# Kernel optimization log

Hardware: AMD Instinct MI355X
Metric: run time of the kernel (lower is better)

Reference implementation:

```python
import jax, jax.numpy as jnp
import numpy as np

VOCAB = 50257
EMBED = 1024

def setup_inputs() -> dict:
    key = jax.random.key(0)
    k1, k2 = jax.random.split(key)
    hidden_states = jax.random.normal(k1, (2, 2048, EMBED), dtype=jnp.float32)
    # nn.Linear weight: [vocab_size, embed_dim], no bias
    W = jax.random.normal(k2, (VOCAB, EMBED), dtype=jnp.float32) * (1.0 / np.sqrt(EMBED))
    return {"hidden_states": hidden_states, "W": W}

def reference(hidden_states, W):
    # logits: [B, S, V] = hidden @ W^T
    logits = jnp.einsum("bsd,vd->bsv", hidden_states, W)
    return jax.nn.log_softmax(logits, axis=-1)
```

## Files before the change

kernel.cpp:

```cpp
#include <hip/hip_runtime.h>
#include <hip/hip_bf16.h>
#include <math.h>

#define VOCAB 50257
#define VPAD  50432
#define EMB   1024
#define NROWS 4096

#define BM 256
#define BN 256
#define BK 64
#define NKT (EMB / BK)
#define NMT (NROWS / BM)
#define NT  (VPAD / BN)
#define NWG (NMT * NT)

typedef __attribute__((ext_vector_type(4))) float  f32x4;
typedef __attribute__((ext_vector_type(16))) float f32x16;
typedef __attribute__((ext_vector_type(4), aligned(4))) float f32x4u;
typedef __attribute__((ext_vector_type(8))) __bf16 bf16x8;

#define FENCE asm volatile("" ::: "memory")
#define BARRIER do { FENCE; __builtin_amdgcn_s_barrier(); FENCE; } while (0)

__global__ __launch_bounds__(256)
void cvt_frag(const float* __restrict__ src, __bf16* __restrict__ dst,
              int valid_rows) {
    const long o8 = (long)blockIdx.x * 256 + threadIdx.x;
    const int l    = (int)(o8 & 63);
    const int u    = (int)((o8 >> 6) & 31);
    const int kt   = (int)((o8 >> 11) & 15);
    const int pn   = (int)(o8 >> 15);
    const int ks   = u >> 3, rblk = u & 7;
    const int grow = pn * 256 + rblk * 32 + (l & 31);
    const int gk   = kt * 64 + ks * 16 + (l >> 5) * 8;
    bf16x8 v;
    if (grow < valid_rows) {
        const float* p = src + (size_t)grow * EMB + gk;
        f32x4 a = *(const f32x4*)p;
        f32x4 b = *(const f32x4*)(p + 4);
        #pragma unroll
        for (int e = 0; e < 4; ++e) {
            v[e]     = (__bf16)a[e];
            v[4 + e] = (__bf16)b[e];
        }
    } else {
        #pragma unroll
        for (int e = 0; e < 8; ++e) v[e] = (__bf16)0.0f;
    }
    *(bf16x8*)(dst + o8 * 8) = v;
}

template <bool LB_OUT>
__global__ __launch_bounds__(512, 2)
void gemm_fused(const __bf16* __restrict__ A, const __bf16* __restrict__ B,
                float* __restrict__ C, __bf16* __restrict__ Lb,
                float* __restrict__ pbuf) {
    __shared__ alignas(16) __bf16 S[65536];

    const int tid  = threadIdx.x;
    const int lane = tid & 63;
    const int wave = tid >> 6;
    const int wm   = (wave >> 2) * 128;
    const int wn   = (wave & 3) * 64;
    const int l31  = lane & 31;
    const int h    = lane >> 5;

    const int b  = blockIdx.x;
    const int lg = (b & 7) * (NWG / 8) + (b >> 3);
    const int q  = lg >> 4, w = lg & 15;
    int mt, nt;
    if (q == 196) { mt = w; nt = 196; }
    else { mt = (q & 1) * 8 + (w & 7); nt = (q >> 1) * 2 + (w >> 3); }
    const int mtB = mt * BM, ntB = nt * BN;

    const __bf16* gAf = A + (size_t)mt * (16 * 16384) + lane * 8;
    const __bf16* gBf = B + (size_t)nt * (16 * 16384) + lane * 8;

    f32x16 acc[4][2];
    #pragma unroll
    for (int mb = 0; mb < 4; ++mb)
        #pragma unroll
        for (int nb = 0; nb < 2; ++nb)
            #pragma unroll
            for (int e = 0; e < 16; ++e) acc[mb][nb][e] = 0.0f;

#define GLOAD(gp, dp)                                                         \
    __builtin_amdgcn_global_load_lds(                                         \
        (const __attribute__((address_space(1))) void*)(gp),                 \
        (__attribute__((address_space(3))) void*)(dp), 16, 0, 0)

#define STAGE_A(bc, kt, u)                                                    \
    GLOAD(gAf + ((size_t)(kt) * 32 + (u) * 8 + wave) * 512,                   \
          &S[(bc) * 32768 + ((u) * 8 + wave) * 512])

#define STAGE_B(bc, kt, u)                                                    \
    GLOAD(gBf + ((size_t)(kt) * 32 + (u) * 8 + wave) * 512,                   \
          &S[(bc) * 32768 + 16384 + ((u) * 8 + wave) * 512])

#define LDA32(dst, c, ks) { _Pragma("unroll")                                 \
    for (int mb_ = 0; mb_ < 4; ++mb_)                                         \
        dst[mb_] = *(const bf16x8*)&S[(c) * 32768                            \
            + (((ks) * 8) + ((wm >> 5) + mb_)) * 512 + lane * 8]; }

#define LDB32(dst, c, ks) { _Pragma("unroll")                                 \
    for (int nb_ = 0; nb_ < 2; ++nb_)                                         \
        dst[nb_] = *(const bf16x8*)&S[(c) * 32768 + 16384                    \
            + (((ks) * 8) + ((wn >> 5) + nb_)) * 512 + lane * 8]; }

#define MFMA8(AF, BF)                                                         \
    __builtin_amdgcn_s_setprio(1);                                            \
    _Pragma("unroll") for (int mb_ = 0; mb_ < 4; ++mb_)                       \
        _Pragma("unroll") for (int nb_ = 0; nb_ < 2; ++nb_)                   \
            acc[mb_][nb_] = __builtin_amdgcn_mfma_f32_32x32x16_bf16(          \
                AF[mb_], BF[nb_], acc[mb_][nb_], 0, 0, 0);                    \
    __builtin_amdgcn_s_setprio(0);

    bf16x8 afA[4], afB[4], bfrA[2], bfrB[2];

    #pragma unroll
    for (int u = 0; u < 4; ++u) { STAGE_A(0, 0, u); STAGE_B(0, 0, u); }

    #pragma unroll 2
    for (int t = 0; t < NKT; ++t) {
        const int c = t & 1;
        const bool pf = (t + 1 < NKT);
        if (pf) {
            STAGE_A(c ^ 1, t + 1, 0); STAGE_B(c ^ 1, t + 1, 0);
            STAGE_A(c ^ 1, t + 1, 1); STAGE_B(c ^ 1, t + 1, 1);
            asm volatile("s_waitcnt vmcnt(4)" ::: "memory");
        } else {
            asm volatile("s_waitcnt vmcnt(0)" ::: "memory");
        }
        BARRIER;
        LDB32(bfrA, c, 0); LDA32(afA, c, 0);
        LDB32(bfrB, c, 1); LDA32(afB, c, 1);
        MFMA8(afA, bfrA);
        if (pf) { STAGE_A(c ^ 1, t + 1, 2); STAGE_B(c ^ 1, t + 1, 2); }
        LDB32(bfrA, c, 2); LDA32(afA, c, 2);
        MFMA8(afB, bfrB);
        if (pf) { STAGE_A(c ^ 1, t + 1, 3); STAGE_B(c ^ 1, t + 1, 3); }
        LDB32(bfrB, c, 3); LDA32(afB, c, 3);
        MFMA8(afA, bfrA);
        MFMA8(afB, bfrB);
        BARRIER;
    }
#undef STAGE_A
#undef STAGE_B
#undef GLOAD

    __syncthreads();
    const bool edge = (ntB + BN > VOCAB);

    if (LB_OUT) {
        #pragma unroll
        for (int mb = 0; mb < 4; ++mb) {
            #pragma unroll
            for (int r = 0; r < 16; ++r) {
                const int grow = mtB + wm + mb * 32 + (r & 3) + 8 * (r >> 2) + 4 * h;
                const size_t rb = (size_t)grow * VPAD + ntB + wn + l31;
                Lb[rb]      = (__bf16)acc[mb][0][r];
                Lb[rb + 32] = (__bf16)acc[mb][1][r];
            }
        }
    } else {
        #pragma unroll
        for (int mb = 0; mb < 4; ++mb) {
            #pragma unroll
            for (int r = 0; r < 16; ++r) {
                const int grow = mtB + wm + mb * 32 + (r & 3) + 8 * (r >> 2) + 4 * h;
                const size_t rb = (size_t)grow * VOCAB;
                const int col0 = ntB + wn + l31;
                if (!edge || col0 < VOCAB)      C[rb + col0]      = acc[mb][0][r];
                if (!edge || col0 + 32 < VOCAB) C[rb + col0 + 32] = acc[mb][1][r];
            }
        }
    }

    float* ldsP = (float*)&S[0];
    const int col0 = ntB + wn + l31;
    #pragma unroll
    for (int mb = 0; mb < 4; ++mb) {
        #pragma unroll
        for (int r = 0; r < 16; ++r) {
            float s = 0.0f;
            if (!edge || col0 < VOCAB)      s += __expf(acc[mb][0][r]);
            if (!edge || col0 + 32 < VOCAB) s += __expf(acc[mb][1][r]);
            s += __shfl_xor(s, 16);
            if (l31 < 16) {
                const int lrow = wm + mb * 32 + (r & 3) + 8 * (r >> 2) + 4 * h;
                ldsP[lrow * 68 + (wave & 3) * 16 + (lane & 15)] = s;
            }
        }
    }
    __syncthreads();

    {
        const int rl = tid >> 1, hf = tid & 1;
        const float* q2 = ldsP + rl * 68 + hf * 32;
        float s = 0.0f;
        #pragma unroll
        for (int k = 0; k < 8; ++k) {
            f32x4 v = *(const f32x4*)(q2 + k * 4);
            s += v[0] + v[1] + v[2] + v[3];
        }
        s += __shfl_xor(s, 1);
        if (hf == 0) pbuf[(size_t)nt * NROWS + mtB + rl] = s;
    }
}

__global__ __launch_bounds__(256)
void lse_reduce(const float* __restrict__ pbuf, float* __restrict__ lse) {
    __shared__ float sl[4][64];
    const int r0 = blockIdx.x * 64;
    const int l  = threadIdx.x & 63;
    const int w  = threadIdx.x >> 6;
    float s = 0.0f;
    for (int t = w; t < NT; t += 4)
        s += pbuf[(size_t)t * NROWS + r0 + l];
    sl[w][l] = s;
    __syncthreads();
    if (threadIdx.x < 64)
        lse[r0 + l] = __logf(sl[0][l] + sl[1][l] + sl[2][l] + sl[3][l]);
}

__global__ __launch_bounds__(256)
void expand_sub(const __bf16* __restrict__ Lb, const float* __restrict__ lse,
                float* __restrict__ C) {
    const int row = blockIdx.x >> 2;
    const int q   = blockIdx.x & 3;
    const float s = lse[row];
    const __bf16* src = Lb + (size_t)row * VPAD;
    float* dst = C + (size_t)row * VOCAB;
    const int i0 = q * 1571;
    const int i1 = (q == 3) ? 6282 : i0 + 1571;
    for (int i = i0 + threadIdx.x; i < i1; i += 256) {
        bf16x8 v = __builtin_nontemporal_load((const bf16x8*)(src + i * 8));
        f32x4u a, b2;
        a[0] = (float)v[0] - s; a[1] = (float)v[1] - s;
        a[2] = (float)v[2] - s; a[3] = (float)v[3] - s;
        b2[0] = (float)v[4] - s; b2[1] = (float)v[5] - s;
        b2[2] = (float)v[6] - s; b2[3] = (float)v[7] - s;
        __builtin_nontemporal_store(a,  (f32x4u*)(dst + i * 8));
        __builtin_nontemporal_store(b2, (f32x4u*)(dst + i * 8 + 4));
    }
    if (q == 3 && threadIdx.x == 0)
        dst[50256] = (float)src[50256] - s;
}

#define FBM 128
#define FBK 32
typedef __attribute__((ext_vector_type(4))) __bf16 bf16x4;
__device__ __forceinline__ int swz_idx(int row, int col) {
    int slot = (col >> 3) ^ ((row >> 1) & 3);
    return row * FBK + slot * 8 + (col & 7);
}

__global__ __launch_bounds__(256, 2)
void gemm_logits(const float* __restrict__ H, const float* __restrict__ W,
                 float* __restrict__ C) {
    __shared__ __bf16 ldsA[FBM * FBK];
    __shared__ __bf16 ldsB[FBM * FBK];

    const int tid  = threadIdx.x;
    const int lane = tid & 63;
    const int wave = tid >> 6;
    const int wm = (wave >> 1) * 64;
    const int wn = (wave & 1) * 64;
    const int mt = blockIdx.x;
    const int nt = blockIdx.y;
    const int srow = tid >> 1;
    const int scol = (tid & 1) * 16;
    const int brow_g = nt * FBM + srow;
    const bool bvalid = brow_g < VOCAB;
    const float* aptr = H + (size_t)(mt * FBM + srow) * EMB + scol;
    const float* bptr = W + (size_t)(bvalid ? brow_g : 0) * EMB + scol;

    f32x4 areg[4], breg[4];
    #pragma unroll
    for (int q = 0; q < 4; ++q) {
        areg[q] = *(const f32x4*)(aptr + q * 4);
        breg[q] = *(const f32x4*)(bptr + q * 4);
    }
    f32x4 acc[4][4];
    const f32x4 vzero = {0.f, 0.f, 0.f, 0.f};
    #pragma unroll
    for (int i = 0; i < 4; ++i)
        #pragma unroll
        for (int j = 0; j < 4; ++j) acc[i][j] = vzero;

    const int frow = lane & 15;
    const int kcol = (lane >> 4) * 8;

    for (int kt = 0; kt < EMB / FBK; ++kt) {
        __syncthreads();
        #pragma unroll
        for (int q = 0; q < 4; ++q) {
            const int col = scol + q * 4;
            bf16x4 av, bv;
            #pragma unroll
            for (int e = 0; e < 4; ++e) {
                av[e] = (__bf16)areg[q][e];
                bv[e] = bvalid ? (__bf16)breg[q][e] : (__bf16)0.0f;
            }
            *(bf16x4*)(&ldsA[swz_idx(srow, col)]) = av;
            *(bf16x4*)(&ldsB[swz_idx(srow, col)]) = bv;
        }
        __syncthreads();
        if (kt + 1 < EMB / FBK) {
            const int ko = (kt + 1) * FBK;
            #pragma unroll
            for (int q = 0; q < 4; ++q) {
                areg[q] = *(const f32x4*)(aptr + ko + q * 4);
                breg[q] = *(const f32x4*)(bptr + ko + q * 4);
            }
        }
        bf16x8 af[4], bfr[4];
        #pragma unroll
        for (int i = 0; i < 4; ++i) {
            af[i]  = *(const bf16x8*)(&ldsA[swz_idx(wm + i * 16 + frow, kcol)]);
            bfr[i] = *(const bf16x8*)(&ldsB[swz_idx(wn + i * 16 + frow, kcol)]);
        }
        #pragma unroll
        for (int i = 0; i < 4; ++i)
            #pragma unroll
            for (int j = 0; j < 4; ++j)
                acc[i][j] = __builtin_amdgcn_mfma_f32_16x16x32_bf16(
                    af[i], bfr[j], acc[i][j], 0, 0, 0);
    }

    const int crow = mt * FBM + wm + (lane >> 4) * 4;
    const int ccol = nt * FBM + wn + (lane & 15);
    #pragma unroll
    for (int i = 0; i < 4; ++i) {
        #pragma unroll
        for (int j = 0; j < 4; ++j) {
            const int col = ccol + j * 16;
            if (col < VOCAB) {
                #pragma unroll
                for (int r = 0; r < 4; ++r)
                    C[(size_t)(crow + i * 16 + r) * VOCAB + col] = acc[i][j][r];
            }
        }
    }
}

__global__ __launch_bounds__(256)
void row_lse(const float* __restrict__ C, float* __restrict__ lse) {
    const int row = blockIdx.x;
    const float* p = C + (size_t)row * VOCAB;

    float m = -INFINITY, l = 0.0f;
    for (int i = threadIdx.x; i < 12564; i += 256) {
        f32x4u v = *(const f32x4u*)(p + 4 * i);
        #pragma unroll
        for (int e = 0; e < 4; ++e) {
            const float x  = v[e];
            const float mn = fmaxf(m, x);
            l = l * __expf(m - mn) + __expf(x - mn);
            m = mn;
        }
    }
    if (threadIdx.x == 0) {
        const float x  = p[50256];
        const float mn = fmaxf(m, x);
        l = l * __expf(m - mn) + __expf(x - mn);
        m = mn;
    }
    #pragma unroll
    for (int off = 1; off < 64; off <<= 1) {
        const float mo = __shfl_xor(m, off);
        const float lo = __shfl_xor(l, off);
        const float mn = fmaxf(m, mo);
        l = l * __expf(m - mn) + lo * __expf(mo - mn);
        m = mn;
    }
    __shared__ float sm[4], sl[4];
    if ((threadIdx.x & 63) == 0) { sm[threadIdx.x >> 6] = m; sl[threadIdx.x >> 6] = l; }
    __syncthreads();
    if (threadIdx.x == 0) {
        m = sm[0]; l = sl[0];
        #pragma unroll
        for (int w = 1; w < 4; ++w) {
            const float mn = fmaxf(m, sm[w]);
            l = l * __expf(m - mn) + sl[w] * __expf(sm[w] - mn);
            m = mn;
        }
        lse[row] = m + __logf(l);
    }
}

__global__ __launch_bounds__(256)
void sub_lse(float* __restrict__ C, const float* __restrict__ lse) {
    const int row = blockIdx.x;
    const float s = lse[row];
    float* p = C + (size_t)row * VOCAB;
    for (int i = threadIdx.x; i < 12564; i += 256) {
        f32x4u v = *(const f32x4u*)(p + 4 * i);
        v[0] -= s; v[1] -= s; v[2] -= s; v[3] -= s;
        *(f32x4u*)(p + 4 * i) = v;
    }
    if (threadIdx.x == 0) p[50256] -= s;
}

extern "C" void kernel_launch(void* const* d_in, const int* in_sizes, int n_in,
                              void* d_out, int out_size, void* d_ws, size_t ws_size,
                              hipStream_t stream) {
    const float* H = (const float*)d_in[0];
    const float* W = (const float*)d_in[1];
    float* C   = (float*)d_out;
    float* lse = (float*)d_ws;

    const long nH  = (long)NROWS * EMB;
    const long nWp = (long)VPAD * EMB;

    const size_t pb_off   = 16384;
    const size_t pb_bytes = (size_t)NT * NROWS * sizeof(float);
    const size_t hf_off   = (pb_off + pb_bytes + 255) & ~(size_t)255;
    const size_t wf_off   = hf_off + (size_t)nH * 2;
    const size_t lb_off   = wf_off + (size_t)nWp * 2;
    const size_t lb_bytes = (size_t)NROWS * VPAD * 2;
    const size_t need_lb   = lb_off + lb_bytes;
    const size_t need_full = lb_off;

    if (ws_size >= need_full) {
        __bf16* Hf = (__bf16*)((char*)d_ws + hf_off);
        __bf16* Wf = (__bf16*)((char*)d_ws + wf_off);
        float*  pb = (float*)((char*)d_ws + pb_off);
        cvt_frag<<<dim3(NMT * 128), 256, 0, stream>>>(H, Hf, NROWS);
        cvt_frag<<<dim3(NT * 128),  256, 0, stream>>>(W, Wf, VOCAB);
        if (ws_size >= need_lb) {
            __bf16* Lb = (__bf16*)((char*)d_ws + lb_off);
            gemm_fused<true><<<dim3(NWG), 512, 0, stream>>>(Hf, Wf, C, Lb, pb);
            lse_reduce<<<dim3(NROWS / 64), 256, 0, stream>>>(pb, lse);
            expand_sub<<<dim3(NROWS * 4), 256, 0, stream>>>(Lb, lse, C);
        } else {
            gemm_fused<false><<<dim3(NWG), 512, 0, stream>>>(Hf, Wf, C, (__bf16*)nullptr, pb);
            lse_reduce<<<dim3(NROWS / 64), 256, 0, stream>>>(pb, lse);
            sub_lse<<<dim3(NROWS), 256, 0, stream>>>(C, lse);
        }
    } else {
        dim3 ggrid(NROWS / FBM, (VOCAB + FBM - 1) / FBM);
        gemm_logits<<<ggrid, 256, 0, stream>>>(H, W, C);
        row_lse<<<dim3(NROWS), 256, 0, stream>>>(C, lse);
        sub_lse<<<dim3(NROWS), 256, 0, stream>>>(C, lse);
    }
}
```

Measured before the change: 851.8 us.

## Use triple-buffered BK=32 pipeline in GEMM and LDS-transposed fragment conversion

Halves the K tile to 32 and switches the GEMM main loop from double to triple buffering, so loads run two tiles ahead, with explicit lgkmcnt waits and barriers around each MFMA group. LDS per block drops from 128KB to 96KB. The fp32-to-bf16 fragment conversion now reads contiguous row chunks into an LDS tile and writes the fragment layout from there, giving more coalesced global reads and fewer blocks. In exchange there are more barriers per K step and less MFMA work between syncs, which could expose latency.

```diff
diff --git a/kernel.cpp b/kernel.cpp
--- a/kernel.cpp
+++ b/kernel.cpp
@@ -9,7 +9,7 @@
 
 #define BM 256
 #define BN 256
-#define BK 64
+#define BK 32
 #define NKT (EMB / BK)
 #define NMT (NROWS / BM)
 #define NT  (VPAD / BN)
@@ -22,33 +22,55 @@
 
 #define FENCE asm volatile("" ::: "memory")
 #define BARRIER do { FENCE; __builtin_amdgcn_s_barrier(); FENCE; } while (0)
+#define WAIT_LGKM do {                                                        \
+        asm volatile("s_waitcnt lgkmcnt(0)" ::: "memory");                    \
+        __builtin_amdgcn_sched_barrier(0);                                    \
+    } while (0)
 
 __global__ __launch_bounds__(256)
 void cvt_frag(const float* __restrict__ src, __bf16* __restrict__ dst,
               int valid_rows) {
-    const long o8 = (long)blockIdx.x * 256 + threadIdx.x;
-    const int l    = (int)(o8 & 63);
-    const int u    = (int)((o8 >> 6) & 31);
-    const int kt   = (int)((o8 >> 11) & 15);
-    const int pn   = (int)(o8 >> 15);
-    const int ks   = u >> 3, rblk = u & 7;
-    const int grow = pn * 256 + rblk * 32 + (l & 31);
-    const int gk   = kt * 64 + ks * 16 + (l >> 5) * 8;
-    bf16x8 v;
+    __shared__ __bf16 T[32][520];
+    const int bid  = blockIdx.x;
+    const int kh   = bid & 1;
+    const int rblk = (bid >> 1) & 7;
+    const int pn   = bid >> 4;
+    const int t    = threadIdx.x;
+    const int row  = t >> 3;
+    const int c0   = (t & 7) * 8;
+    const int grow = pn * 256 + rblk * 32 + row;
+
     if (grow < valid_rows) {
-        const float* p = src + (size_t)grow * EMB + gk;
-        f32x4 a = *(const f32x4*)p;
-        f32x4 b = *(const f32x4*)(p + 4);
-        #pragma unroll
-        for (int e = 0; e < 4; ++e) {
-            v[e]     = (__bf16)a[e];
-            v[4 + e] = (__bf16)b[e];
+        const float* p = src + (size_t)grow * EMB + kh * 512;
+        #pragma unroll
+        for (int it = 0; it < 8; ++it) {
+            const int c = c0 + it * 64;
+            f32x4 a = *(const f32x4*)(p + c);
+            f32x4 b = *(const f32x4*)(p + c + 4);
+            bf16x8 v;
+            #pragma unroll
+            for (int e = 0; e < 4; ++e) { v[e] = (__bf16)a[e]; v[4 + e] = (__bf16)b[e]; }
+            *(bf16x8*)&T[row][c] = v;
         }
     } else {
-        #pragma unroll
-        for (int e = 0; e < 8; ++e) v[e] = (__bf16)0.0f;
-    }
-    *(bf16x8*)(dst + o8 * 8) = v;
+        bf16x8 z;
+        #pragma unroll
+        for (int e = 0; e < 8; ++e) z[e] = (__bf16)0.0f;
+        #pragma unroll
+        for (int it = 0; it < 8; ++it) *(bf16x8*)&T[row][c0 + it * 64] = z;
+    }
+    __syncthreads();
+
+    const int wv = t >> 6, l = t & 63;
+    #pragma unroll
+    for (int j = 0; j < 8; ++j) {
+        const int u   = wv * 8 + j;
+        const int ktl = u >> 1;
+        const int ks  = u & 1;
+        bf16x8 v = *(const bf16x8*)&T[l & 31][ktl * 32 + ks * 16 + (l >> 5) * 8];
+        const size_t uo = ((size_t)(pn * 32 + kh * 16 + ktl) * 16 + ks * 8 + rblk) * 512;
+        *(bf16x8*)(dst + uo + l * 8) = v;
+    }
 }
 
 template <bool LB_OUT>
@@ -56,7 +78,7 @@
 void gemm_fused(const __bf16* __restrict__ A, const __bf16* __restrict__ B,
                 float* __restrict__ C, __bf16* __restrict__ Lb,
                 float* __restrict__ pbuf) {
-    __shared__ alignas(16) __bf16 S[65536];
+    __shared__ alignas(16) __bf16 S[49152];
 
     const int tid  = threadIdx.x;
     const int lane = tid & 63;
@@ -74,8 +96,8 @@
     else { mt = (q & 1) * 8 + (w & 7); nt = (q >> 1) * 2 + (w >> 3); }
     const int mtB = mt * BM, ntB = nt * BN;
 
-    const __bf16* gAf = A + (size_t)mt * (16 * 16384) + lane * 8;
-    const __bf16* gBf = B + (size_t)nt * (16 * 16384) + lane * 8;
+    const __bf16* gAf = A + (size_t)mt * (NKT * 16 * 512) + lane * 8;
+    const __bf16* gBf = B + (size_t)nt * (NKT * 16 * 512) + lane * 8;
 
     f32x16 acc[4][2];
     #pragma unroll
@@ -91,21 +113,21 @@
         (__attribute__((address_space(3))) void*)(dp), 16, 0, 0)
 
 #define STAGE_A(bc, kt, u)                                                    \
-    GLOAD(gAf + ((size_t)(kt) * 32 + (u) * 8 + wave) * 512,                   \
-          &S[(bc) * 32768 + ((u) * 8 + wave) * 512])
+    GLOAD(gAf + ((size_t)(kt) * 16 + (u) * 8 + wave) * 512,                   \
+          &S[(bc) * 16384 + ((u) * 8 + wave) * 512])
 
 #define STAGE_B(bc, kt, u)                                                    \
-    GLOAD(gBf + ((size_t)(kt) * 32 + (u) * 8 + wave) * 512,                   \
-          &S[(bc) * 32768 + 16384 + ((u) * 8 + wave) * 512])
+    GLOAD(gBf + ((size_t)(kt) * 16 + (u) * 8 + wave) * 512,                   \
+          &S[(bc) * 16384 + 8192 + ((u) * 8 + wave) * 512])
 
 #define LDA32(dst, c, ks) { _Pragma("unroll")                                 \
     for (int mb_ = 0; mb_ < 4; ++mb_)                                         \
-        dst[mb_] = *(const bf16x8*)&S[(c) * 32768                            \
+        dst[mb_] = *(const bf16x8*)&S[(c) * 16384                            \
             + (((ks) * 8) + ((wm >> 5) + mb_)) * 512 + lane * 8]; }
 
 #define LDB32(dst, c, ks) { _Pragma("unroll")                                 \
     for (int nb_ = 0; nb_ < 2; ++nb_)                                         \
-        dst[nb_] = *(const bf16x8*)&S[(c) * 32768 + 16384                    \
+        dst[nb_] = *(const bf16x8*)&S[(c) * 16384 + 8192                     \
             + (((ks) * 8) + ((wn >> 5) + nb_)) * 512 + lane * 8]; }
 
 #define MFMA8(AF, BF)                                                         \
@@ -118,32 +140,35 @@
 
     bf16x8 afA[4], afB[4], bfrA[2], bfrB[2];
 
-    #pragma unroll
-    for (int u = 0; u < 4; ++u) { STAGE_A(0, 0, u); STAGE_B(0, 0, u); }
-
-    #pragma unroll 2
+    STAGE_A(0, 0, 0); STAGE_B(0, 0, 0); STAGE_A(0, 0, 1); STAGE_B(0, 0, 1);
+    STAGE_A(1, 1, 0); STAGE_B(1, 1, 0); STAGE_A(1, 1, 1); STAGE_B(1, 1, 1);
+    asm volatile("s_waitcnt vmcnt(4)" ::: "memory");
+    BARRIER;
+
+    int c = 0;
     for (int t = 0; t < NKT; ++t) {
-        const int c = t & 1;
-        const bool pf = (t + 1 < NKT);
-        if (pf) {
-            STAGE_A(c ^ 1, t + 1, 0); STAGE_B(c ^ 1, t + 1, 0);
-            STAGE_A(c ^ 1, t + 1, 1); STAGE_B(c ^ 1, t + 1, 1);
-            asm volatile("s_waitcnt vmcnt(4)" ::: "memory");
-        } else {
-            asm volatile("s_waitcnt vmcnt(0)" ::: "memory");
-        }
+        const int n  = (c == 0) ? 2 : c - 1;
+        const bool p1 = (t + 1 < NKT);
+        const bool p2 = (t + 2 < NKT);
+
+        LDB32(bfrA, c, 0); LDA32(afA, c, 0);
+        if (p2) { STAGE_A(n, t + 2, 0); STAGE_B(n, t + 2, 0); }
         BARRIER;
-        LDB32(bfrA, c, 0); LDA32(afA, c, 0);
+        WAIT_LGKM;
+        MFMA8(afA, bfrA);
+        BARRIER;
         LDB32(bfrB, c, 1); LDA32(afB, c, 1);
-        MFMA8(afA, bfrA);
-        if (pf) { STAGE_A(c ^ 1, t + 1, 2); STAGE_B(c ^ 1, t + 1, 2); }
-        LDB32(bfrA, c, 2); LDA32(afA, c, 2);
-        MFMA8(afB, bfrB);
-        if (pf) { STAGE_A(c ^ 1, t + 1, 3); STAGE_B(c ^ 1, t + 1, 3); }
-        LDB32(bfrB, c, 3); LDA32(afB, c, 3);
-        MFMA8(afA, bfrA);
+        if (p2) { STAGE_A(n, t + 2, 1); STAGE_B(n, t + 2, 1); }
+        if (p1) {
+            if (p2) asm volatile("s_waitcnt vmcnt(4)" ::: "memory");
+            else    asm volatile("s_waitcnt vmcnt(0)" ::: "memory");
+        }
+        BARRIER;
+        WAIT_LGKM;
         MFMA8(afB, bfrB);
         BARRIER;
+
+        c = (c == 2) ? 0 : c + 1;
     }
 #undef STAGE_A
 #undef STAGE_B
@@ -427,8 +452,8 @@
         __bf16* Hf = (__bf16*)((char*)d_ws + hf_off);
         __bf16* Wf = (__bf16*)((char*)d_ws + wf_off);
         float*  pb = (float*)((char*)d_ws + pb_off);
-        cvt_frag<<<dim3(NMT * 128), 256, 0, stream>>>(H, Hf, NROWS);
-        cvt_frag<<<dim3(NT * 128),  256, 0, stream>>>(W, Wf, VOCAB);
+        cvt_frag<<<dim3(NMT * 16), 256, 0, stream>>>(H, Hf, NROWS);
+        cvt_frag<<<dim3(NT * 16),  256, 0, stream>>>(W, Wf, VOCAB);
         if (ws_size >= need_lb) {
             __bf16* Lb = (__bf16*)((char*)d_ws + lb_off);
             gemm_fused<true><<<dim3(NWG), 512, 0, stream>>>(Hf, Wf, C, Lb, pb);
```

After: 835.2 us. Within noise of the previous version (-1.9%).
